# Kernel tuning notes

Hardware: AMD Instinct MI355X
Metric: run time of the kernel (lower is better)

The kernel has to match this reference:

```python
import jax, jax.numpy as jnp
import numpy as np

B, T, I, H = 128, 64, 128, 256
UNFOLDS = 6
EPS = 1e-08


def setup_inputs() -> dict:
    key = jax.random.key(0)
    ks = jax.random.split(key, 12)
    u = lambda k, sh, lo, hi: jax.random.uniform(k, sh, minval=lo, maxval=hi, dtype=jnp.float32)
    return {
        "x": jax.random.normal(ks[0], (B, T, I), dtype=jnp.float32),
        "input_weight": jnp.ones((I,), jnp.float32),
        "input_bias": jnp.zeros((I,), jnp.float32),
        "sensing_mu": u(ks[1], (I, H), 0.3, 0.8),
        "sensing_sigma": u(ks[2], (I, H), 3.0, 8.0),
        "sensing_w": u(ks[3], (I, H), 0.01, 1.0),
        "sensing_erev": 2.0 * jax.random.randint(ks[4], (I, H), 0, 2).astype(jnp.float32) - 1.0,
        "internal_mu": u(ks[5], (H, H), 0.3, 0.8),
        "internal_sigma": u(ks[6], (H, H), 3.0, 8.0),
        "internal_w": u(ks[7], (H, H), 0.01, 1.0),
        "internal_erev": 2.0 * jax.random.randint(ks[8], (H, H), 0, 2).astype(jnp.float32) - 1.0,
        "vleak": u(ks[9], (H,), -0.2, 0.2),
        "gleak": jnp.ones((H,), jnp.float32),
        "cm": jnp.ones((H,), jnp.float32) * 0.5,
        "output_weight": jnp.ones((H,), jnp.float32),
        "output_bias": jnp.zeros((H,), jnp.float32),
    }


def _gate(V, mu, sigma):
    # torch: sigmoid(sigma * (V.unsqueeze(-1) - mu)); V:[B,D] -> [B,D,H]
    return jax.nn.sigmoid(sigma * (V[..., None] - mu))


def reference(x, input_weight, input_bias, sensing_mu, sensing_sigma, sensing_w,
              sensing_erev, internal_mu, internal_sigma, internal_w, internal_erev,
              vleak, gleak, cm, output_weight, output_bias):
    # time_elapsed = 1.0 default -> cm_t = cm / (1/UNFOLDS) = cm * UNFOLDS
    cm_t = cm * UNFOLDS
    gl_vl = gleak * vleak

    def step(V, xt):
        # affine input mapping
        xm = xt * input_weight + input_bias                      # [B, I]
        s_act = sensing_w * _gate(xm, sensing_mu, sensing_sigma)  # [B, I, H]
        w_num_s = jnp.einsum('bih,ih->bh', s_act, sensing_erev)   # sum over I
        w_den_s = s_act.sum(axis=1)                               # [B, H]

        def unfold(Vc, _):
            w_act = internal_w * _gate(Vc, internal_mu, internal_sigma)  # [B, H, H]
            w_num = jnp.einsum('bij,ij->bj', w_act, internal_erev) + w_num_s
            w_den = w_act.sum(axis=1) + w_den_s
            Vn = (Vc * cm_t + gl_vl + w_num) / (cm_t + gleak + w_den + EPS)
            return Vn, None

        V, _ = jax.lax.scan(unfold, V, None, length=UNFOLDS)
        out_t = V * output_weight + output_bias
        return V, out_t

    h0 = jnp.zeros((x.shape[0], cm.shape[0]), x.dtype)
    hT, out = jax.lax.scan(step, h0, jnp.swapaxes(x, 0, 1))  # scan over T
    return jnp.swapaxes(out, 0, 1), hT  # ([B, T, H], [B, H])
```

## Files before the change

### kernel.cpp

```cpp
#include <hip/hip_runtime.h>
#include <hip/hip_fp16.h>

#define B_ 128
#define T_ 64
#define I_ 128
#define H_ 256
#define UF 6
#define EPSF 1e-8f

typedef _Float16 f16x2 __attribute__((ext_vector_type(2)));
union H2U { __half2 h; f16x2 v; unsigned u; };

static __device__ __forceinline__ float rcpf(float x) { return __builtin_amdgcn_rcpf(x); }

#define GATE2(VW, AK, BK, WK, NM, DN) {                        \
    H2U v2_; v2_.u = (VW);                                     \
    H2U av_; av_.u = (AK);                                     \
    H2U bv_; bv_.u = (BK);                                     \
    __half2 z_ = __hfma2(av_.h, v2_.h, bv_.h);                 \
    __half2 e_ = h2exp2(z_);                                   \
    __half2 s_ = __hadd2(e_, __float2half2_rn(1.0f));          \
    H2U rv_; rv_.h = h2rcp(s_);                                \
    H2U ws_; ws_.u = (WK);                                     \
    H2U wa_; wa_.u = ws_.u & 0x7fff7fffu;                      \
    NM = __builtin_amdgcn_fdot2(ws_.v, rv_.v, NM, false);      \
    DN = __builtin_amdgcn_fdot2(wa_.v, rv_.v, DN, false);      \
}

__global__ __launch_bounds__(256) void pack_params(
    const float* __restrict__ smu, const float* __restrict__ ssig,
    const float* __restrict__ sw,  const float* __restrict__ serev,
    const float* __restrict__ imu, const float* __restrict__ isig,
    const float* __restrict__ iw,  const float* __restrict__ ierev,
    uint2* __restrict__ ABp, unsigned* __restrict__ Wp,
    uint2* __restrict__ SAB, unsigned* __restrict__ SW,
    unsigned* __restrict__ Vg4)
{
    const float L2E = 1.4426950408889634f;
    int idx = blockIdx.x * 256 + threadIdx.x;
    int r = idx >> 8, jg = idx & 255;
    {
        int i0 = 2 * r, i1 = i0 + 1;
        unsigned a0 = __half_as_ushort(__float2half_rn(-isig[i0 * H_ + jg] * L2E));
        unsigned a1 = __half_as_ushort(__float2half_rn(-isig[i1 * H_ + jg] * L2E));
        unsigned b0 = __half_as_ushort(__float2half_rn(isig[i0 * H_ + jg] * imu[i0 * H_ + jg] * L2E));
        unsigned b1 = __half_as_ushort(__float2half_rn(isig[i1 * H_ + jg] * imu[i1 * H_ + jg] * L2E));
        ABp[idx] = make_uint2(a0 | (a1 << 16), b0 | (b1 << 16));
        unsigned w0 = __half_as_ushort(__float2half_rn(iw[i0 * H_ + jg] * ierev[i0 * H_ + jg]));
        unsigned w1 = __half_as_ushort(__float2half_rn(iw[i1 * H_ + jg] * ierev[i1 * H_ + jg]));
        Wp[idx] = w0 | (w1 << 16);
    }
    if (idx < 64 * H_) {
        int i0 = 2 * r, i1 = i0 + 1;
        unsigned a0 = __half_as_ushort(__float2half_rn(-ssig[i0 * H_ + jg] * L2E));
        unsigned a1 = __half_as_ushort(__float2half_rn(-ssig[i1 * H_ + jg] * L2E));
        unsigned b0 = __half_as_ushort(__float2half_rn(ssig[i0 * H_ + jg] * smu[i0 * H_ + jg] * L2E));
        unsigned b1 = __half_as_ushort(__float2half_rn(ssig[i1 * H_ + jg] * smu[i1 * H_ + jg] * L2E));
        SAB[idx] = make_uint2(a0 | (a1 << 16), b0 | (b1 << 16));
        unsigned w0 = __half_as_ushort(__float2half_rn(sw[i0 * H_ + jg] * serev[i0 * H_ + jg]));
        unsigned w1 = __half_as_ushort(__float2half_rn(sw[i1 * H_ + jg] * serev[i1 * H_ + jg]));
        SW[idx] = w0 | (w1 << 16);
    }
    Vg4[idx] = 0u;
    Vg4[idx + 32768] = 0u;
}

__global__ __launch_bounds__(1024)
__attribute__((amdgpu_waves_per_eu(4, 4)))
void ltc_rec(
    const float* __restrict__ x, const float* __restrict__ in_w, const float* __restrict__ in_b,
    const uint2* __restrict__ ABp, const unsigned* __restrict__ Wp,
    const uint2* __restrict__ SAB, const unsigned* __restrict__ SW,
    const float* __restrict__ vleak, const float* __restrict__ gleak, const float* __restrict__ cm,
    const float* __restrict__ out_w, const float* __restrict__ out_b,
    unsigned* __restrict__ Vg4,
    float* __restrict__ out, float* __restrict__ hT)
{
    __shared__ __align__(16) unsigned V2u[H_ / 2];
    __shared__ __align__(16) unsigned xs2[I_ / 2];

    const int bx  = blockIdx.x;
    const int b   = bx & 127;
    const int jh  = bx >> 7;
    const int tid = threadIdx.x;
    const int c   = tid & 7;
    const int j   = tid >> 3;
    const int jg  = (jh << 7) + j;
    const int pjbase = ((jh ^ 1) << 7);
    const int BH  = B_ * H_;

    unsigned ra[16], rb[16], rw[16];
    unsigned sa[8], sb[8], sw8[8];
    {
        const int po = (jh << 6) + (c << 3);
        const int pp = ((jh ^ 1) << 6) + (c << 3);
        const int ps = (c << 3);
        #pragma unroll
        for (int k = 0; k < 8; ++k) {
            uint2 u0 = ABp[((po + k) << 8) + jg];
            ra[k] = u0.x; rb[k] = u0.y; rw[k] = Wp[((po + k) << 8) + jg];
            uint2 u1 = ABp[((pp + k) << 8) + jg];
            ra[8 + k] = u1.x; rb[8 + k] = u1.y; rw[8 + k] = Wp[((pp + k) << 8) + jg];
            uint2 u2 = SAB[((ps + k) << 8) + jg];
            sa[k] = u2.x; sb[k] = u2.y; sw8[k] = SW[((ps + k) << 8) + jg];
        }
    }

    const float cmt  = cm[jg] * (float)UF;
    const float gl   = gleak[jg];
    const float glvl = gl * vleak[jg];
    const float dc   = cmt + gl + EPSF;
    const float owj  = out_w[jg], obj = out_b[jg];
    float iw0 = 0.f, iw1 = 0.f, ib0 = 0.f, ib1 = 0.f;
    if (tid < 64) { iw0 = in_w[2 * tid]; iw1 = in_w[2 * tid + 1];
                    ib0 = in_b[2 * tid]; ib1 = in_b[2 * tid + 1]; }
    if (tid < H_ / 2) V2u[tid] = 0u;
    float vreg = 0.f;

    const float* xrow = x + (size_t)b * (T_ * I_);

    for (int t = 0; t < T_; ++t) {
        if (tid < 64) {
            float2 xv = *reinterpret_cast<const float2*>(xrow + t * I_ + 2 * tid);
            __half2 hh = __floats2half2_rn(fmaf(xv.x, iw0, ib0), fmaf(xv.y, iw1, ib1));
            H2U u; u.h = hh; xs2[tid] = u.u;
        }
        __syncthreads();

        float qsn = 0.f, qsd = 0.f;
        {
            const uint4 xa = *reinterpret_cast<const uint4*>(xs2 + (c << 3));
            const uint4 xb = *reinterpret_cast<const uint4*>(xs2 + (c << 3) + 4);
            GATE2(xa.x, sa[0], sb[0], sw8[0], qsn, qsd);
            GATE2(xa.y, sa[1], sb[1], sw8[1], qsn, qsd);
            GATE2(xa.z, sa[2], sb[2], sw8[2], qsn, qsd);
            GATE2(xa.w, sa[3], sb[3], sw8[3], qsn, qsd);
            GATE2(xb.x, sa[4], sb[4], sw8[4], qsn, qsd);
            GATE2(xb.y, sa[5], sb[5], sw8[5], qsn, qsd);
            GATE2(xb.z, sa[6], sb[6], sw8[6], qsn, qsd);
            GATE2(xb.w, sa[7], sb[7], sw8[7], qsn, qsd);
        }

        for (int u = 0; u < UF; ++u) {
            const int p = t * UF + u + 1;
            float nm = qsn, dn = qsd;

            unsigned pv = 0; const unsigned* src = nullptr; unsigned want = 0;
            if (p > 1 && tid < 128) {
                want = (unsigned)(p - 1);
                src = Vg4 + (size_t)(want & 1) * BH + (b << 8) + pjbase + tid;
                pv = __hip_atomic_load(src, __ATOMIC_RELAXED, __HIP_MEMORY_SCOPE_AGENT);
            }

            {
                const int vb = (jh << 6) + (c << 3);
                const uint4 va = *reinterpret_cast<const uint4*>(V2u + vb);
                const uint4 vb4 = *reinterpret_cast<const uint4*>(V2u + vb + 4);
                GATE2(va.x,  ra[0], rb[0], rw[0], nm, dn);
                GATE2(va.y,  ra[1], rb[1], rw[1], nm, dn);
                GATE2(va.z,  ra[2], rb[2], rw[2], nm, dn);
                GATE2(va.w,  ra[3], rb[3], rw[3], nm, dn);
                GATE2(vb4.x, ra[4], rb[4], rw[4], nm, dn);
                GATE2(vb4.y, ra[5], rb[5], rw[5], nm, dn);
                GATE2(vb4.z, ra[6], rb[6], rw[6], nm, dn);
                GATE2(vb4.w, ra[7], rb[7], rw[7], nm, dn);
            }

            if (p > 1 && tid < 128) {
                while ((pv >> 16) != want)
                    pv = __hip_atomic_load(src, __ATOMIC_RELAXED, __HIP_MEMORY_SCOPE_AGENT);
                unsigned hv = pv & 0xffffu;
                unsigned hv1 = (unsigned)__shfl_down((int)hv, 1);
                if (!(tid & 1)) V2u[(pjbase >> 1) + (tid >> 1)] = hv | (hv1 << 16);
            }
            __syncthreads();

            {
                const int vb = ((jh ^ 1) << 6) + (c << 3);
                const uint4 va = *reinterpret_cast<const uint4*>(V2u + vb);
                const uint4 vb4 = *reinterpret_cast<const uint4*>(V2u + vb + 4);
                GATE2(va.x,  ra[8],  rb[8],  rw[8],  nm, dn);
                GATE2(va.y,  ra[9],  rb[9],  rw[9],  nm, dn);
                GATE2(va.z,  ra[10], rb[10], rw[10], nm, dn);
                GATE2(va.w,  ra[11], rb[11], rw[11], nm, dn);
                GATE2(vb4.x, ra[12], rb[12], rw[12], nm, dn);
                GATE2(vb4.y, ra[13], rb[13], rw[13], nm, dn);
                GATE2(vb4.z, ra[14], rb[14], rw[14], nm, dn);
                GATE2(vb4.w, ra[15], rb[15], rw[15], nm, dn);
            }

            nm += __shfl_xor(nm, 1); dn += __shfl_xor(dn, 1);
            nm += __shfl_xor(nm, 2); dn += __shfl_xor(dn, 2);
            nm += __shfl_xor(nm, 4); dn += __shfl_xor(dn, 4);

            float Vn = (fmaf(vreg, cmt, glvl) + nm) * rcpf(dn + dc);
            vreg = Vn;
            unsigned h0 = __half_as_ushort(__float2half_rn(Vn));
            if (c == 0)
                __hip_atomic_store(Vg4 + (size_t)(p & 1) * BH + (b << 8) + jg,
                                   ((unsigned)p << 16) | h0,
                                   __ATOMIC_RELAXED, __HIP_MEMORY_SCOPE_AGENT);
            unsigned h1 = (unsigned)__shfl_down((int)h0, 8);
            if (c == 0 && !(j & 1)) V2u[jg >> 1] = h0 | (h1 << 16);
            __syncthreads();
        }

        if (c == 0) out[((size_t)b * T_ + t) * H_ + jg] = fmaf(vreg, owj, obj);
    }
    if (c == 0) hT[(b << 8) + jg] = vreg;
}

extern "C" void kernel_launch(void* const* d_in, const int* in_sizes, int n_in,
                              void* d_out, int out_size, void* d_ws, size_t ws_size,
                              hipStream_t stream) {
    const float* x     = (const float*)d_in[0];
    const float* in_w  = (const float*)d_in[1];
    const float* in_b  = (const float*)d_in[2];
    const float* smu   = (const float*)d_in[3];
    const float* ssig  = (const float*)d_in[4];
    const float* sw    = (const float*)d_in[5];
    const float* serev = (const float*)d_in[6];
    const float* imu   = (const float*)d_in[7];
    const float* isig  = (const float*)d_in[8];
    const float* iw    = (const float*)d_in[9];
    const float* ierev = (const float*)d_in[10];
    const float* vleak = (const float*)d_in[11];
    const float* gleak = (const float*)d_in[12];
    const float* cmv   = (const float*)d_in[13];
    const float* ow    = (const float*)d_in[14];
    const float* ob    = (const float*)d_in[15];

    float* out = (float*)d_out;
    float* hT  = out + (size_t)B_ * T_ * H_;

    char* w = (char*)d_ws;
    uint2*    ABp = (uint2*)(w);
    unsigned* Wp  = (unsigned*)(w + (256 << 10));
    uint2*    SAB = (uint2*)(w + (384 << 10));
    unsigned* SW  = (unsigned*)(w + (512 << 10));
    unsigned* Vg4 = (unsigned*)(w + (576 << 10));

    pack_params<<<dim3(128), dim3(256), 0, stream>>>(
        smu, ssig, sw, serev, imu, isig, iw, ierev, ABp, Wp, SAB, SW, Vg4);

    ltc_rec<<<dim3(256), dim3(1024), 0, stream>>>(
        x, in_w, in_b, ABp, Wp, SAB, SW, vleak, gleak, cmv, ow, ob,
        Vg4, out, hT);
}
```

Baseline: 1.024 ms.

## Replace sigmoid exp/rcp with LDS lookup table and stage gate params in LDS

The packed-fp16 exp2 and reciprocal sigmoid is replaced by a 1024-entry fp16 sigmoid table in LDS, indexed via a clamped, scaled fp32 FMA and a magic-number float-to-int trick. The internal mu/sigma coefficients move from registers into a swizzled 128KB LDS buffer, freeing VGPRs. Sensing coefficients are now read from global memory on every timestep. The goal is to cut transcendental ALU work in the recurrent inner loop. In exchange it adds LDS gather traffic, possible bank conflicts, scalar fp32 gate math in place of packed half2, and a table-quantization accuracy risk.

```diff
diff --git a/kernel.cpp b/kernel.cpp
--- a/kernel.cpp
+++ b/kernel.cpp
@@ -7,24 +7,31 @@
 #define H_ 256
 #define UF 6
 #define EPSF 1e-8f
+#define SCL 85.3333333f
 
 typedef _Float16 f16x2 __attribute__((ext_vector_type(2)));
 union H2U { __half2 h; f16x2 v; unsigned u; };
 
 static __device__ __forceinline__ float rcpf(float x) { return __builtin_amdgcn_rcpf(x); }
-
-#define GATE2(VW, AK, BK, WK, NM, DN) {                        \
-    H2U v2_; v2_.u = (VW);                                     \
-    H2U av_; av_.u = (AK);                                     \
-    H2U bv_; bv_.u = (BK);                                     \
-    __half2 z_ = __hfma2(av_.h, v2_.h, bv_.h);                 \
-    __half2 e_ = h2exp2(z_);                                   \
-    __half2 s_ = __hadd2(e_, __float2half2_rn(1.0f));          \
-    H2U rv_; rv_.h = h2rcp(s_);                                \
-    H2U ws_; ws_.u = (WK);                                     \
-    H2U wa_; wa_.u = ws_.u & 0x7fff7fffu;                      \
-    NM = __builtin_amdgcn_fdot2(ws_.v, rv_.v, NM, false);      \
-    DN = __builtin_amdgcn_fdot2(wa_.v, rv_.v, DN, false);      \
+static __device__ __forceinline__ unsigned f2h(float f) { return (unsigned)__half_as_ushort(__float2half_rn(f)); }
+
+#define GPAIR(ABU, VW, WU, NM, DN) {                                            \
+    H2U a_; a_.u = (ABU).x;                                                     \
+    H2U b_; b_.u = (ABU).y;                                                     \
+    H2U v_; v_.u = (VW);                                                        \
+    float z0_ = fmaf(__half2float(__low2half(a_.h)),  __half2float(__low2half(v_.h)),  __half2float(__low2half(b_.h)));  \
+    float z1_ = fmaf(__half2float(__high2half(a_.h)), __half2float(__high2half(v_.h)), __half2float(__high2half(b_.h))); \
+    z0_ = __builtin_amdgcn_fmed3f(z0_, cLO, cHI);                               \
+    z1_ = __builtin_amdgcn_fmed3f(z1_, cLO, cHI);                               \
+    unsigned i0_ = __float_as_uint(z0_ + 8389632.0f) & 0x7FEu;                  \
+    unsigned i1_ = __float_as_uint(z1_ + 8389632.0f) & 0x7FEu;                  \
+    __half r0_ = *(const __half*)(Lb + i0_);                                    \
+    __half r1_ = *(const __half*)(Lb + i1_);                                    \
+    H2U r_; r_.h = __halves2half2(r0_, r1_);                                    \
+    H2U w_; w_.u = (WU);                                                        \
+    H2U wa_; wa_.u = w_.u & 0x7fff7fffu;                                        \
+    NM = __builtin_amdgcn_fdot2(w_.v, r_.v, NM, false);                         \
+    DN = __builtin_amdgcn_fdot2(wa_.v, r_.v, DN, false);                        \
 }
 
 __global__ __launch_bounds__(256) void pack_params(
@@ -32,34 +39,42 @@
     const float* __restrict__ sw,  const float* __restrict__ serev,
     const float* __restrict__ imu, const float* __restrict__ isig,
     const float* __restrict__ iw,  const float* __restrict__ ierev,
-    uint2* __restrict__ ABp, unsigned* __restrict__ Wp,
-    uint2* __restrict__ SAB, unsigned* __restrict__ SW,
+    uint2* __restrict__ ABg, unsigned* __restrict__ Wg,
+    uint2* __restrict__ SABg, unsigned* __restrict__ SWg,
     unsigned* __restrict__ Vg4)
 {
-    const float L2E = 1.4426950408889634f;
+    const float K = 1.4426950408889634f * SCL;
     int idx = blockIdx.x * 256 + threadIdx.x;
-    int r = idx >> 8, jg = idx & 255;
-    {
-        int i0 = 2 * r, i1 = i0 + 1;
-        unsigned a0 = __half_as_ushort(__float2half_rn(-isig[i0 * H_ + jg] * L2E));
-        unsigned a1 = __half_as_ushort(__float2half_rn(-isig[i1 * H_ + jg] * L2E));
-        unsigned b0 = __half_as_ushort(__float2half_rn(isig[i0 * H_ + jg] * imu[i0 * H_ + jg] * L2E));
-        unsigned b1 = __half_as_ushort(__float2half_rn(isig[i1 * H_ + jg] * imu[i1 * H_ + jg] * L2E));
-        ABp[idx] = make_uint2(a0 | (a1 << 16), b0 | (b1 << 16));
-        unsigned w0 = __half_as_ushort(__float2half_rn(iw[i0 * H_ + jg] * ierev[i0 * H_ + jg]));
-        unsigned w1 = __half_as_ushort(__float2half_rn(iw[i1 * H_ + jg] * ierev[i1 * H_ + jg]));
-        Wp[idx] = w0 | (w1 << 16);
+    {
+        int jh = idx >> 14, rest = idx & 16383;
+        int P = rest >> 7, jcol = rest & 127;
+        int j = jcol ^ (((P >> 3) & 7) << 1);
+        int jg = (jh << 7) + j;
+        int i0 = 2 * P, i1 = i0 + 1;
+        unsigned a0 = f2h(-isig[i0 * H_ + jg] * K);
+        unsigned a1 = f2h(-isig[i1 * H_ + jg] * K);
+        unsigned b0 = f2h(isig[i0 * H_ + jg] * imu[i0 * H_ + jg] * K);
+        unsigned b1 = f2h(isig[i1 * H_ + jg] * imu[i1 * H_ + jg] * K);
+        ABg[idx] = make_uint2(a0 | (a1 << 16), b0 | (b1 << 16));
+    }
+    {
+        int P = idx >> 8, jg = idx & 255;
+        int i0 = 2 * P, i1 = i0 + 1;
+        unsigned w0 = f2h(iw[i0 * H_ + jg] * ierev[i0 * H_ + jg]);
+        unsigned w1 = f2h(iw[i1 * H_ + jg] * ierev[i1 * H_ + jg]);
+        Wg[idx] = w0 | (w1 << 16);
     }
     if (idx < 64 * H_) {
-        int i0 = 2 * r, i1 = i0 + 1;
-        unsigned a0 = __half_as_ushort(__float2half_rn(-ssig[i0 * H_ + jg] * L2E));
-        unsigned a1 = __half_as_ushort(__float2half_rn(-ssig[i1 * H_ + jg] * L2E));
-        unsigned b0 = __half_as_ushort(__float2half_rn(ssig[i0 * H_ + jg] * smu[i0 * H_ + jg] * L2E));
-        unsigned b1 = __half_as_ushort(__float2half_rn(ssig[i1 * H_ + jg] * smu[i1 * H_ + jg] * L2E));
-        SAB[idx] = make_uint2(a0 | (a1 << 16), b0 | (b1 << 16));
-        unsigned w0 = __half_as_ushort(__float2half_rn(sw[i0 * H_ + jg] * serev[i0 * H_ + jg]));
-        unsigned w1 = __half_as_ushort(__float2half_rn(sw[i1 * H_ + jg] * serev[i1 * H_ + jg]));
-        SW[idx] = w0 | (w1 << 16);
+        int p = idx >> 8, jg = idx & 255;
+        int i0 = 2 * p, i1 = i0 + 1;
+        unsigned a0 = f2h(-ssig[i0 * H_ + jg] * K);
+        unsigned a1 = f2h(-ssig[i1 * H_ + jg] * K);
+        unsigned b0 = f2h(ssig[i0 * H_ + jg] * smu[i0 * H_ + jg] * K);
+        unsigned b1 = f2h(ssig[i1 * H_ + jg] * smu[i1 * H_ + jg] * K);
+        SABg[idx] = make_uint2(a0 | (a1 << 16), b0 | (b1 << 16));
+        unsigned w0 = f2h(sw[i0 * H_ + jg] * serev[i0 * H_ + jg]);
+        unsigned w1 = f2h(sw[i1 * H_ + jg] * serev[i1 * H_ + jg]);
+        SWg[idx] = w0 | (w1 << 16);
     }
     Vg4[idx] = 0u;
     Vg4[idx + 32768] = 0u;
@@ -69,15 +84,18 @@
 __attribute__((amdgpu_waves_per_eu(4, 4)))
 void ltc_rec(
     const float* __restrict__ x, const float* __restrict__ in_w, const float* __restrict__ in_b,
-    const uint2* __restrict__ ABp, const unsigned* __restrict__ Wp,
-    const uint2* __restrict__ SAB, const unsigned* __restrict__ SW,
+    const uint2* __restrict__ ABg, const unsigned* __restrict__ Wg,
+    const uint2* __restrict__ SABg, const unsigned* __restrict__ SWg,
     const float* __restrict__ vleak, const float* __restrict__ gleak, const float* __restrict__ cm,
     const float* __restrict__ out_w, const float* __restrict__ out_b,
     unsigned* __restrict__ Vg4,
     float* __restrict__ out, float* __restrict__ hT)
 {
-    __shared__ __align__(16) unsigned V2u[H_ / 2];
-    __shared__ __align__(16) unsigned xs2[I_ / 2];
+    __shared__ __align__(16) unsigned char L[133888];
+    __half* tbl = (__half*)L;
+    const char* Lb = (const char*)L;
+    unsigned* V2u = (unsigned*)(L + 133120);
+    unsigned* xs2 = (unsigned*)(L + 133632);
 
     const int bx  = blockIdx.x;
     const int b   = bx & 127;
@@ -86,23 +104,30 @@
     const int c   = tid & 7;
     const int j   = tid >> 3;
     const int jg  = (jh << 7) + j;
-    const int pjbase = ((jh ^ 1) << 7);
+    const int pjbase = (jh ^ 1) << 7;
     const int BH  = B_ * H_;
 
-    unsigned ra[16], rb[16], rw[16];
-    unsigned sa[8], sb[8], sw8[8];
+    {
+        float z = ((float)(2 * tid) + 0.5f - 1024.0f) * (1.0f / SCL);
+        tbl[tid] = __float2half_rn(rcpf(1.0f + exp2f(z)));
+    }
+
+    {
+        const uint4* src = (const uint4*)(ABg + ((size_t)jh << 14));
+        uint4* dst = (uint4*)(L + 2048);
+        #pragma unroll
+        for (int k = 0; k < 8; ++k) dst[tid + (k << 10)] = src[tid + (k << 10)];
+    }
+
+    unsigned rw[16], sw8[8];
     {
         const int po = (jh << 6) + (c << 3);
         const int pp = ((jh ^ 1) << 6) + (c << 3);
-        const int ps = (c << 3);
         #pragma unroll
         for (int k = 0; k < 8; ++k) {
-            uint2 u0 = ABp[((po + k) << 8) + jg];
-            ra[k] = u0.x; rb[k] = u0.y; rw[k] = Wp[((po + k) << 8) + jg];
-            uint2 u1 = ABp[((pp + k) << 8) + jg];
-            ra[8 + k] = u1.x; rb[8 + k] = u1.y; rw[8 + k] = Wp[((pp + k) << 8) + jg];
-            uint2 u2 = SAB[((ps + k) << 8) + jg];
-            sa[k] = u2.x; sb[k] = u2.y; sw8[k] = SW[((ps + k) << 8) + jg];
+            rw[k]     = Wg[((po + k) << 8) + jg];
+            rw[8 + k] = Wg[((pp + k) << 8) + jg];
+            sw8[k]    = SWg[(((c << 3) + k) << 8) + jg];
         }
     }
 
@@ -114,31 +139,37 @@
     float iw0 = 0.f, iw1 = 0.f, ib0 = 0.f, ib1 = 0.f;
     if (tid < 64) { iw0 = in_w[2 * tid]; iw1 = in_w[2 * tid + 1];
                     ib0 = in_b[2 * tid]; ib1 = in_b[2 * tid + 1]; }
-    if (tid < H_ / 2) V2u[tid] = 0u;
+    if (tid < 128) V2u[tid] = 0u;
     float vreg = 0.f;
 
+    const float cLO = -1023.0f, cHI = 1022.5f;
     const float* xrow = x + (size_t)b * (T_ * I_);
+
+    const int colb = (j ^ (c << 1)) << 3;
+    const char* abA = (const char*)L + 2048 + ((((jh << 6) + (c << 3))) << 10) + colb;
+    const char* abB = (const char*)L + 2048 + (((((jh ^ 1) << 6)) + (c << 3)) << 10) + colb;
+    const int vbaseA = (jh << 6) + (c << 3);
+    const int vbaseB = ((jh ^ 1) << 6) + (c << 3);
+    const uint2* sabBase = SABg + (((c << 3)) << 8) + jg;
 
     for (int t = 0; t < T_; ++t) {
         if (tid < 64) {
-            float2 xv = *reinterpret_cast<const float2*>(xrow + t * I_ + 2 * tid);
-            __half2 hh = __floats2half2_rn(fmaf(xv.x, iw0, ib0), fmaf(xv.y, iw1, ib1));
-            H2U u; u.h = hh; xs2[tid] = u.u;
+            float2 xv = *(const float2*)(xrow + t * I_ + 2 * tid);
+            H2U u_; u_.h = __floats2half2_rn(fmaf(xv.x, iw0, ib0), fmaf(xv.y, iw1, ib1));
+            xs2[tid] = u_.u;
         }
         __syncthreads();
 
         float qsn = 0.f, qsd = 0.f;
         {
-            const uint4 xa = *reinterpret_cast<const uint4*>(xs2 + (c << 3));
-            const uint4 xb = *reinterpret_cast<const uint4*>(xs2 + (c << 3) + 4);
-            GATE2(xa.x, sa[0], sb[0], sw8[0], qsn, qsd);
-            GATE2(xa.y, sa[1], sb[1], sw8[1], qsn, qsd);
-            GATE2(xa.z, sa[2], sb[2], sw8[2], qsn, qsd);
-            GATE2(xa.w, sa[3], sb[3], sw8[3], qsn, qsd);
-            GATE2(xb.x, sa[4], sb[4], sw8[4], qsn, qsd);
-            GATE2(xb.y, sa[5], sb[5], sw8[5], qsn, qsd);
-            GATE2(xb.z, sa[6], sb[6], sw8[6], qsn, qsd);
-            GATE2(xb.w, sa[7], sb[7], sw8[7], qsn, qsd);
+            const uint4 xa = *(const uint4*)(xs2 + (c << 3));
+            const uint4 xb = *(const uint4*)(xs2 + (c << 3) + 4);
+            #pragma unroll
+            for (int k = 0; k < 8; ++k) {
+                uint2 sab = sabBase[k << 8];
+                unsigned xw = (k < 4) ? ((const unsigned*)&xa)[k] : ((const unsigned*)&xb)[k - 4];
+                GPAIR(sab, xw, sw8[k], qsn, qsd);
+            }
         }
 
         for (int u = 0; u < UF; ++u) {
@@ -153,17 +184,14 @@
             }
 
             {
-                const int vb = (jh << 6) + (c << 3);
-                const uint4 va = *reinterpret_cast<const uint4*>(V2u + vb);
-                const uint4 vb4 = *reinterpret_cast<const uint4*>(V2u + vb + 4);
-                GATE2(va.x,  ra[0], rb[0], rw[0], nm, dn);
-                GATE2(va.y,  ra[1], rb[1], rw[1], nm, dn);
-                GATE2(va.z,  ra[2], rb[2], rw[2], nm, dn);
-                GATE2(va.w,  ra[3], rb[3], rw[3], nm, dn);
-                GATE2(vb4.x, ra[4], rb[4], rw[4], nm, dn);
-                GATE2(vb4.y, ra[5], rb[5], rw[5], nm, dn);
-                GATE2(vb4.z, ra[6], rb[6], rw[6], nm, dn);
-                GATE2(vb4.w, ra[7], rb[7], rw[7], nm, dn);
+                const uint4 va = *(const uint4*)(V2u + vbaseA);
+                const uint4 vb = *(const uint4*)(V2u + vbaseA + 4);
+                #pragma unroll
+                for (int k = 0; k < 8; ++k) {
+                    uint2 ab = *(const uint2*)(abA + (k << 10));
+                    unsigned vw = (k < 4) ? ((const unsigned*)&va)[k] : ((const unsigned*)&vb)[k - 4];
+                    GPAIR(ab, vw, rw[k], nm, dn);
+                }
             }
 
             if (p > 1 && tid < 128) {
@@ -176,17 +204,14 @@
             __syncthreads();
 
             {
-                const int vb = ((jh ^ 1) << 6) + (c << 3);
-                const uint4 va = *reinterpret_cast<const uint4*>(V2u + vb);
-                const uint4 vb4 = *reinterpret_cast<const uint4*>(V2u + vb + 4);
-                GATE2(va.x,  ra[8],  rb[8],  rw[8],  nm, dn);
-                GATE2(va.y,  ra[9],  rb[9],  rw[9],  nm, dn);
-                GATE2(va.z,  ra[10], rb[10], rw[10], nm, dn);
-                GATE2(va.w,  ra[11], rb[11], rw[11], nm, dn);
-                GATE2(vb4.x, ra[12], rb[12], rw[12], nm, dn);
-                GATE2(vb4.y, ra[13], rb[13], rw[13], nm, dn);
-                GATE2(vb4.z, ra[14], rb[14], rw[14], nm, dn);
-                GATE2(vb4.w, ra[15], rb[15], rw[15], nm, dn);
+                const uint4 va = *(const uint4*)(V2u + vbaseB);
+                const uint4 vb = *(const uint4*)(V2u + vbaseB + 4);
+                #pragma unroll
+                for (int k = 0; k < 8; ++k) {
+                    uint2 ab = *(const uint2*)(abB + (k << 10));
+                    unsigned vw = (k < 4) ? ((const unsigned*)&va)[k] : ((const unsigned*)&vb)[k - 4];
+                    GPAIR(ab, vw, rw[8 + k], nm, dn);
+                }
             }
 
             nm += __shfl_xor(nm, 1); dn += __shfl_xor(dn, 1);
@@ -195,7 +220,7 @@
 
             float Vn = (fmaf(vreg, cmt, glvl) + nm) * rcpf(dn + dc);
             vreg = Vn;
-            unsigned h0 = __half_as_ushort(__float2half_rn(Vn));
+            unsigned h0 = (unsigned)__half_as_ushort(__float2half_rn(Vn));
             if (c == 0)
                 __hip_atomic_store(Vg4 + (size_t)(p & 1) * BH + (b << 8) + jg,
                                    ((unsigned)p << 16) | h0,
@@ -234,16 +259,16 @@
     float* hT  = out + (size_t)B_ * T_ * H_;
 
     char* w = (char*)d_ws;
-    uint2*    ABp = (uint2*)(w);
-    unsigned* Wp  = (unsigned*)(w + (256 << 10));
-    uint2*    SAB = (uint2*)(w + (384 << 10));
-    unsigned* SW  = (unsigned*)(w + (512 << 10));
-    unsigned* Vg4 = (unsigned*)(w + (576 << 10));
+    uint2*    ABg  = (uint2*)(w);
+    unsigned* Wg   = (unsigned*)(w + (256 << 10));
+    uint2*    SABg = (uint2*)(w + (384 << 10));
+    unsigned* SWg  = (unsigned*)(w + (512 << 10));
+    unsigned* Vg4  = (unsigned*)(w + (576 << 10));
 
     pack_params<<<dim3(128), dim3(256), 0, stream>>>(
-        smu, ssig, sw, serev, imu, isig, iw, ierev, ABp, Wp, SAB, SW, Vg4);
+        smu, ssig, sw, serev, imu, isig, iw, ierev, ABg, Wg, SABg, SWg, Vg4);
 
     ltc_rec<<<dim3(256), dim3(1024), 0, stream>>>(
-        x, in_w, in_b, ABp, Wp, SAB, SW, vleak, gleak, cmv, ow, ob,
+        x, in_w, in_b, ABg, Wg, SABg, SWg, vleak, gleak, cmv, ow, ob,
         Vg4, out, hT);
 }
```

Measured after the change: 1.029 ms. No clear change (+0.5%).
